# Optimization experiments

Measured on AMD Instinct MI355X. Metric: run time of the kernel, lower is better.

Reference implementation:

```python
import jax, jax.numpy as jnp
from jax import lax
import numpy as np

B, S, D, H = 64, 256, 1024, 1024
NEG = -1e9


def setup_inputs() -> dict:
    key = jax.random.key(0)
    ks = jax.random.split(key, 8)
    sd = 1.0 / np.sqrt(D)
    sh = 1.0 / np.sqrt(H + 1)
    return {
        "lstm_features": jax.random.normal(ks[0], (B, S, D), jnp.float32),
        "mask": jnp.ones((B, S), jnp.int32),
        "Wl": jax.random.normal(ks[1], (D, H), jnp.float32) * sd,
        "bl": jnp.zeros((H,), jnp.float32),
        "Wr": jax.random.normal(ks[2], (D, H), jnp.float32) * sd,
        "br": jnp.zeros((H,), jnp.float32),
        "Wbil": jax.random.normal(ks[3], (H + 1, H + 1), jnp.float32) * sh,
        "bbil": jnp.zeros((), jnp.float32),
    }


def _span_scores(lstm_features, Wl, bl, Wr, br, Wbil, bbil):
    # left/right MLPs: Linear + LeakyReLU(0.1) (dropout=0 at inference)
    lefts = jax.nn.leaky_relu(lstm_features @ Wl + bl, 0.1)   # [B,S,H]
    rights = jax.nn.leaky_relu(lstm_features @ Wr + br, 0.1)  # [B,S,H]
    ones = jnp.ones(lefts.shape[:-1] + (1,), lefts.dtype)
    l1 = jnp.concatenate([lefts, ones], axis=-1)   # [B,S,H+1] (use_input_biases=True)
    r1 = jnp.concatenate([rights, ones], axis=-1)
    # bilinear: l1 @ W @ r1^T + bias  -> [B,S,S]
    return jnp.einsum('bsh,hg,btg->bst', l1, Wbil, r1) + bbil


def _cky(scores):
    """CKY over one [S,S] score matrix. chart[i,j]=scores[i,j]+max_s chart[i,s]+chart[s+1,j];
    singleton spans score 0. Returns (chart, best-split table)."""
    n = scores.shape[0]
    idx = jnp.arange(n)
    m = jnp.arange(n - 1)  # split offsets
    chart0 = jnp.zeros((n, n), scores.dtype)
    split0 = jnp.zeros((n, n), jnp.int32)

    def step(carry, w):
        chart, split = carry
        j = idx + w
        jc = jnp.clip(j, 0, n - 1)
        li = jnp.clip(idx[:, None] + m[None, :], 0, n - 1)       # left end
        ri = jnp.clip(idx[:, None] + m[None, :] + 1, 0, n - 1)   # right start
        cand = chart[idx[:, None], li] + chart[ri, jc[:, None]]  # [n, n-1]
        valid = (m[None, :] < w) & (j[:, None] < n)
        cand = jnp.where(valid, cand, NEG)
        val = scores[idx, jc] + jnp.max(cand, axis=1)
        bsplit = (idx + jnp.argmax(cand, axis=1)).astype(jnp.int32)
        ok = j < n
        chart = chart.at[idx, jc].set(jnp.where(ok, val, chart[idx, jc]))
        split = split.at[idx, jc].set(jnp.where(ok, bsplit, split[idx, jc]))
        return (chart, split), None

    (chart, split), _ = lax.scan(step, (chart0, split0), jnp.arange(1, n))
    return chart, split


def _backtrack(split):
    """Extract the n-1 internal spans of the best tree (fixed-size stack, jit-safe)."""
    n = split.shape[0]
    stack = jnp.full((2 * n, 2), -1, jnp.int32).at[0].set(jnp.array([0, n - 1], jnp.int32))
    out = jnp.zeros((n, 2), jnp.int32)

    def body(t, state):
        def do_pop(st):
            stack, top, out, cnt = st
            ij = stack[top - 1]
            i, j = ij[0], ij[1]
            top = top - 1
            out = out.at[cnt].set(ij)
            cnt = cnt + 1
            s = split[i, j]
            stack = stack.at[top].set(jnp.stack([i, s]))          # left child
            top = top + (s > i).astype(jnp.int32)
            stack = stack.at[top].set(jnp.stack([s + 1, j]))      # right child
            top = top + (j > s + 1).astype(jnp.int32)
            return (stack, top, out, cnt)
        return lax.cond(state[1] > 0, do_pop, lambda s: s, state)

    state = (stack, jnp.int32(1), out, jnp.int32(0))
    _, _, out, _ = lax.fori_loop(0, n - 1, body, state)
    return out  # [n,2] (lefts, rights), zero-padded like torch.zeros in original


def reference(lstm_features, mask, Wl, bl, Wr, br, Wbil, bbil):
    scores = _span_scores(lstm_features, Wl, bl, Wr, br, Wbil, bbil)  # [B,S,S]
    _, split = jax.vmap(_cky)(scores)
    spans = jax.vmap(_backtrack)(split)  # [B,S,2]
    ret_lefts = spans[..., 0].astype(jnp.int64)
    ret_rights = spans[..., 1].astype(jnp.int64)
    return ret_lefts, ret_rights
```

## Files before the change

kernel.cpp:

```cpp
#include <hip/hip_runtime.h>
#include <cstdint>


#define Bb 64
#define Ss 256
#define Dd 1024
#define Hh 1024

typedef __attribute__((ext_vector_type(8))) _Float16 f16x8;
typedef __attribute__((ext_vector_type(4))) float f32x4;

__device__ __forceinline__ void split2(float x, unsigned short& h,
                                       unsigned short& l) {
  _Float16 hh = (_Float16)x;
  _Float16 ll = (_Float16)(x - (float)hh);
  h = __builtin_bit_cast(unsigned short, hh);
  l = __builtin_bit_cast(unsigned short, ll);
}

__device__ __forceinline__ void gl_lds16(const void* g, void* l) {
  __builtin_amdgcn_global_load_lds(
      (const __attribute__((address_space(1))) void*)g,
      (__attribute__((address_space(3))) void*)l, 16, 0, 0);
}

__global__ __launch_bounds__(256) void splitw_kernel(
    const float* __restrict__ W, int ldw, unsigned short* __restrict__ O,
    long long plane) {
  int idx = blockIdx.x * 256 + threadIdx.x;
  int n = idx >> 10, k = idx & 1023;
  float x = W[(long long)k * ldw + n];
  unsigned short h, l;
  split2(x, h, l);
  O[idx] = h;
  O[plane + idx] = l;
}

__global__ __launch_bounds__(256) void bilvec_kernel(
    const float* __restrict__ Wbil, float* __restrict__ brow,
    float* __restrict__ bcol, float* __restrict__ corner) {
  int i = blockIdx.x * 256 + threadIdx.x;
  brow[i] = Wbil[1024 * 1025 + i];
  bcol[i] = Wbil[i * 1025 + 1024];
  if (i == 0) corner[0] = Wbil[1024 * 1025 + 1024];
}

__device__ __forceinline__ void pack8(char* dst, const unsigned short* v) {
  uint4 u;
  u.x = (unsigned)v[0] | ((unsigned)v[1] << 16);
  u.y = (unsigned)v[2] | ((unsigned)v[3] << 16);
  u.z = (unsigned)v[4] | ((unsigned)v[5] << 16);
  u.w = (unsigned)v[6] | ((unsigned)v[7] << 16);
  *(uint4*)dst = u;
}

__device__ __forceinline__ void split_store16f(const float* xs, char* lds,
                                               int base, int wa0, int wa1) {
  unsigned short hs[16], ls[16];
#pragma unroll
  for (int i = 0; i < 16; ++i) split2(xs[i], hs[i], ls[i]);
  pack8(&lds[base + wa0], hs);
  pack8(&lds[base + wa1], hs + 8);
  pack8(&lds[base + 8192 + wa0], ls);
  pack8(&lds[base + 8192 + wa1], ls + 8);
}

#define MFMA4(afv, bh, blv, accs, nf)                                        \
  {                                                                          \
    _Pragma("unroll") for (int mf = 0; mf < 4; ++mf) accs[mf][nf] =          \
        __builtin_amdgcn_mfma_f32_16x16x32_f16(afv[0][mf], bh,               \
                                               accs[mf][nf], 0, 0, 0);       \
    _Pragma("unroll") for (int mf = 0; mf < 4; ++mf) accs[mf][nf] =          \
        __builtin_amdgcn_mfma_f32_16x16x32_f16(afv[0][mf], blv,              \
                                               accs[mf][nf], 0, 0, 0);       \
    _Pragma("unroll") for (int mf = 0; mf < 4; ++mf) accs[mf][nf] =          \
        __builtin_amdgcn_mfma_f32_16x16x32_f16(afv[1][mf], bh,               \
                                               accs[mf][nf], 0, 0, 0);       \
    _Pragma("unroll") for (int mf = 0; mf < 4; ++mf) accs[mf][nf] =          \
        __builtin_amdgcn_mfma_f32_16x16x32_f16(afv[1][mf], blv,              \
                                               accs[mf][nf], 0, 0, 0);       \
  }

template <bool LEAKY>
__global__ __launch_bounds__(256, 3) void gemm_mfma_kernel(
    const float* __restrict__ A, const unsigned short* __restrict__ Bsp,
    long long bplane, float* __restrict__ C0, float* __restrict__ C1,
    const float* __restrict__ bias0, const float* __restrict__ bias1) {
  const int m0 = blockIdx.y * 128;
  const int n0 = blockIdx.x * 128;
  __shared__ __align__(16) char lds[49152];
  const int t = threadIdx.x;
  const int L = t & 63, w = t >> 6, q = L >> 4, l15 = L & 15;

  const int ar = t >> 1, ah = t & 1;
  const float* aptr = A + (long long)(m0 + ar) * 1024 + ah * 16;
  const int phiA = ((ar >> 1) ^ (ar >> 3)) & 3;
  const int wa0 = ar * 64 + (((2 * ah + 0) ^ phiA) << 4);
  const int wa1 = ar * 64 + (((2 * ah + 1) ^ phiA) << 4);

  int offA0[4], offB0[4];
#pragma unroll
  for (int f = 0; f < 4; ++f) {
    int rowa = ((w & 1) << 6) + (f << 4) + l15;
    offA0[f] = rowa * 64 + ((q ^ (((rowa >> 1) ^ (rowa >> 3)) & 3)) << 4);
    int rowb = ((w >> 1) << 6) + (f << 4) + l15;
    offB0[f] = rowb * 64 + ((q ^ (((rowb >> 1) ^ (rowb >> 3)) & 3)) << 4);
  }

  const int lrow = L >> 2, lchk = L & 3;
  const unsigned short* bsrc[4];
  int bldso[4];
#pragma unroll
  for (int i = 0; i < 4; ++i) {
    int O = ((w << 2) + i) << 10;
    int s2 = O >> 13;
    int r = ((O & 8191) >> 6) + lrow;
    int phi = ((r >> 1) ^ (r >> 3)) & 3;
    bsrc[i] = Bsp + (long long)s2 * bplane + (long long)(n0 + r) * 1024 +
              ((lchk ^ phi) << 3);
    bldso[i] = O;
  }

  f32x4 acc[4][4];
#pragma unroll
  for (int i = 0; i < 4; ++i)
#pragma unroll
    for (int j = 0; j < 4; ++j) acc[i][j] = (f32x4){0.f, 0.f, 0.f, 0.f};

#pragma unroll
  for (int i = 0; i < 4; ++i) gl_lds16(bsrc[i], &lds[16384 + bldso[i]]);
  float4 a0 = *(const float4*)(aptr + 0);
  float4 a1 = *(const float4*)(aptr + 4);
  float4 a2 = *(const float4*)(aptr + 8);
  float4 a3 = *(const float4*)(aptr + 12);

  int cur = 0;
  for (int k0 = 0; k0 < 1024; k0 += 32) {
    {
      float xs[16] = {a0.x, a0.y, a0.z, a0.w, a1.x, a1.y, a1.z, a1.w,
                      a2.x, a2.y, a2.z, a2.w, a3.x, a3.y, a3.z, a3.w};
      split_store16f(xs, lds, 0, wa0, wa1);
    }
    asm volatile("s_waitcnt vmcnt(0) lgkmcnt(0)\n\ts_barrier" ::: "memory");
    if (k0 < 992) {
      a0 = *(const float4*)(aptr + k0 + 32);
      a1 = *(const float4*)(aptr + k0 + 36);
      a2 = *(const float4*)(aptr + k0 + 40);
      a3 = *(const float4*)(aptr + k0 + 44);
      const int bn = 16384 + ((cur ^ 1) << 14);
#pragma unroll
      for (int i = 0; i < 4; ++i)
        gl_lds16(bsrc[i] + k0 + 32, &lds[bn + bldso[i]]);
    }
    const int bb = 16384 + (cur << 14);
    f16x8 af[2][4];
#pragma unroll
    for (int s = 0; s < 2; ++s)
#pragma unroll
      for (int f = 0; f < 4; ++f)
        af[s][f] = *(const f16x8*)&lds[s * 8192 + offA0[f]];
#pragma unroll
    for (int nf = 0; nf < 4; ++nf) {
      f16x8 bh = *(const f16x8*)&lds[bb + offB0[nf]];
      f16x8 bl = *(const f16x8*)&lds[bb + 8192 + offB0[nf]];
      MFMA4(af, bh, bl, acc, nf);
    }
    asm volatile("s_waitcnt lgkmcnt(0)\n\ts_barrier" ::: "memory");
    cur ^= 1;
  }

  const bool isR = (n0 >= 1024);
  float* Co = isR ? C1 : C0;
  const float* bp = isR ? bias1 : bias0;
  const int nc0 = n0 & 1023;
#pragma unroll
  for (int nf = 0; nf < 4; ++nf) {
    int col = nc0 + ((w >> 1) << 6) + (nf << 4) + l15;
    float bz = bp[col];
#pragma unroll
    for (int mf = 0; mf < 4; ++mf) {
#pragma unroll
      for (int r = 0; r < 4; ++r) {
        int row = m0 + ((w & 1) << 6) + (mf << 4) + (q << 2) + r;
        float x = acc[mf][nf][r] + bz;
        if (LEAKY) x = (x > 0.f) ? x : 0.1f * x;
        Co[(long long)row * 1024 + col] = x;
      }
    }
  }
}

__global__ __launch_bounds__(256, 3) void gemmnt_mfma_kernel(
    const float* __restrict__ A, const float* __restrict__ B,
    float* __restrict__ C, const float* __restrict__ rowAdd,
    const float* __restrict__ scal) {
  const int bz = blockIdx.z;
  A += (long long)bz * 256 * 1024;
  B += (long long)bz * 256 * 1024;
  C += (long long)bz * 256 * 256;
  const int m0 = blockIdx.y * 128;
  const int n0 = blockIdx.x * 128;
  __shared__ __align__(16) char lds[32768];
  const int t = threadIdx.x;
  const int L = t & 63, w = t >> 6, q = L >> 4, l15 = L & 15;

  const int ar = t >> 1, ah = t & 1;
  const float* aptr = A + (long long)(m0 + ar) * 1024 + ah * 16;
  const float* bptr = B + (long long)(n0 + ar) * 1024 + ah * 16;
  const int phiA = ((ar >> 1) ^ (ar >> 3)) & 3;
  const int wa0 = ar * 64 + (((2 * ah + 0) ^ phiA) << 4);
  const int wa1 = ar * 64 + (((2 * ah + 1) ^ phiA) << 4);

  int offA0[4], offB0[4];
#pragma unroll
  for (int f = 0; f < 4; ++f) {
    int rowa = ((w & 1) << 6) + (f << 4) + l15;
    offA0[f] = rowa * 64 + ((q ^ (((rowa >> 1) ^ (rowa >> 3)) & 3)) << 4);
    int rowb = ((w >> 1) << 6) + (f << 4) + l15;
    offB0[f] =
        16384 + rowb * 64 + ((q ^ (((rowb >> 1) ^ (rowb >> 3)) & 3)) << 4);
  }

  f32x4 acc[4][4];
#pragma unroll
  for (int i = 0; i < 4; ++i)
#pragma unroll
    for (int j = 0; j < 4; ++j) acc[i][j] = (f32x4){0.f, 0.f, 0.f, 0.f};

  float4 a0 = *(const float4*)(aptr + 0);
  float4 a1 = *(const float4*)(aptr + 4);
  float4 a2 = *(const float4*)(aptr + 8);
  float4 a3 = *(const float4*)(aptr + 12);
  float4 b0 = *(const float4*)(bptr + 0);
  float4 b1 = *(const float4*)(bptr + 4);
  float4 b2 = *(const float4*)(bptr + 8);
  float4 b3 = *(const float4*)(bptr + 12);

  for (int k0 = 0; k0 < 1024; k0 += 32) {
    {
      float xs[16] = {a0.x, a0.y, a0.z, a0.w, a1.x, a1.y, a1.z, a1.w,
                      a2.x, a2.y, a2.z, a2.w, a3.x, a3.y, a3.z, a3.w};
      split_store16f(xs, lds, 0, wa0, wa1);
      float ys[16] = {b0.x, b0.y, b0.z, b0.w, b1.x, b1.y, b1.z, b1.w,
                      b2.x, b2.y, b2.z, b2.w, b3.x, b3.y, b3.z, b3.w};
      split_store16f(ys, lds, 16384, wa0, wa1);
    }
    asm volatile("s_waitcnt lgkmcnt(0)\n\ts_barrier" ::: "memory");
    if (k0 < 992) {
      a0 = *(const float4*)(aptr + k0 + 32);
      a1 = *(const float4*)(aptr + k0 + 36);
      a2 = *(const float4*)(aptr + k0 + 40);
      a3 = *(const float4*)(aptr + k0 + 44);
      b0 = *(const float4*)(bptr + k0 + 32);
      b1 = *(const float4*)(bptr + k0 + 36);
      b2 = *(const float4*)(bptr + k0 + 40);
      b3 = *(const float4*)(bptr + k0 + 44);
    }
    f16x8 af[2][4];
#pragma unroll
    for (int s = 0; s < 2; ++s)
#pragma unroll
      for (int f = 0; f < 4; ++f)
        af[s][f] = *(const f16x8*)&lds[s * 8192 + offA0[f]];
#pragma unroll
    for (int nf = 0; nf < 4; ++nf) {
      f16x8 bh = *(const f16x8*)&lds[offB0[nf]];
      f16x8 bl = *(const f16x8*)&lds[8192 + offB0[nf]];
      MFMA4(af, bh, bl, acc, nf);
    }
    asm volatile("s_waitcnt lgkmcnt(0)\n\ts_barrier" ::: "memory");
  }

  const float sc_add = scal[0];
#pragma unroll
  for (int mf = 0; mf < 4; ++mf) {
#pragma unroll
    for (int r = 0; r < 4; ++r) {
      int row = m0 + ((w & 1) << 6) + (mf << 4) + (q << 2) + r;
      float radd = sc_add + rowAdd[(long long)bz * 256 + row];
#pragma unroll
      for (int nf = 0; nf < 4; ++nf) {
        int col = n0 + ((w >> 1) << 6) + (nf << 4) + l15;
        C[(long long)row * 256 + col] = acc[mf][nf][r] + radd;
      }
    }
  }
}

__global__ __launch_bounds__(64) void colvec_kernel(
    const float* __restrict__ lefts, const float* __restrict__ bcol,
    const float* __restrict__ corner, float* __restrict__ tmpb) {
  int row = blockIdx.x;
  int lane = threadIdx.x;
  const float* a = lefts + (long long)row * Hh;
  float s = 0.f;
#pragma unroll
  for (int h = lane; h < Hh; h += 64) s = fmaf(a[h], bcol[h], s);
#pragma unroll
  for (int off = 32; off > 0; off >>= 1) s += __shfl_down(s, off, 64);
  if (lane == 0) tmpb[row] = s + corner[0];
}

__global__ __launch_bounds__(1024) void cky_kernel(
    const float* __restrict__ scores,
    uint8_t* __restrict__ Sws,
    int* __restrict__ out)
{
  const int b = blockIdx.x;
  const int t = threadIdx.x;
  const int n = Ss;
  const float* sc = scores + (long long)b * n * n;
  uint8_t* SP = Sws + (long long)b * 32896;

  __shared__ float Dch[32896];
  __shared__ float pv[2][2048];
  __shared__ uint8_t pmv[2][2048];
  __shared__ int stk[256];

  const int offT[16] = {0,    256,  511,  765,  1018, 1270, 1521, 1771,
                        2020, 2268, 2515, 2761, 3006, 3250, 3493, 3735};

  if (t < n) {
    out[b * n + t] = 0;
    out[Bb * n + b * n + t] = 0;
    Dch[t] = 0.f;
  }
  pv[1][t] = -3.0e38f;
  pv[1][t + 1024] = -3.0e38f;

  float PS[16];
  PS[0] = 0.f;
#pragma unroll
  for (int w = 1; w <= 15; ++w) {
    int ic = t;
    if (ic > 255 - w) ic = 255 - w;
    PS[w] = sc[ic * 257 + w];
  }
  asm volatile("s_waitcnt lgkmcnt(0)\n\ts_barrier" ::: "memory");

#pragma unroll
  for (int w = 1; w <= 15; ++w) {
    if (t < 256 - w) {
      float bb = Dch[offT[w - 1] + t + 1];
      int bm = 0;
#pragma unroll
      for (int m = 1; m < 15; ++m) {
        if (m >= w) break;
        float c = Dch[offT[m] + t] + Dch[offT[w - 1 - m] + t + m + 1];
        if (c > bb) { bb = c; bm = m; }
      }
      Dch[offT[w] + t] = PS[w] + bb;
      SP[offT[w] + t] = (uint8_t)bm;
    }
    asm volatile("s_waitcnt lgkmcnt(0)\n\ts_barrier" ::: "memory");
  }

  auto run_b = [&](int W0b, int pbuf) {
    const int cnv = n - W0b - 8;
    int jb, gb, u, delta;
    if (cnv > 128) {
      jb = 7 - (t >> 7);
      gb = 0;
      u = t & 127;
      delta = 128;
    } else {
      const int wid = t >> 6;
      jb = 7 - (wid >> 1);
      gb = wid & 1;
      u = t & 63;
      delta = (cnv > 64) ? 64 : 0;
    }
    const int Wb = W0b + 8 + jb;
    const int nvb = n - Wb;
    int cnt = W0b - jb - 8;
    if (cnt < 0) cnt = 0;
    const int mlo = jb + 8;
    int ml, mh;
    if (cnv > 128) {
      ml = mlo;
      mh = mlo + cnt;
    } else {
      const int per = (cnt + 1) >> 1;
      ml = mlo + gb * per;
      mh = mlo + cnt;
      int e = ml + per;
      if (e < mh) mh = e;
    }
    float b0 = -3.0e38f, b1 = -3.0e38f;
    int m0i = ml, m1i = ml;
    if (u < nvb && ml < mh) {
      int al = ml * n - ((ml * (ml - 1)) >> 1) + u;
      const int kr = Wb - 1 - ml;
      int ar = kr * n - ((kr * (kr - 1)) >> 1) + u + ml + 1;
      int dl = n - ml;
      int dr = n - Wb + ml + 1;
      if (delta) {
#pragma unroll 4
        for (int m = ml; m < mh; ++m) {
          float l0 = Dch[al], l1 = Dch[al + delta];
          float r0 = Dch[ar], r1 = Dch[ar + delta];
          float c0 = l0 + r0, c1 = l1 + r1;
          if (c0 > b0) { b0 = c0; m0i = m; }
          if (c1 > b1) { b1 = c1; m1i = m; }
          al += dl;
          ar -= dr;
          --dl;
          ++dr;
        }
      } else {
#pragma unroll 8
        for (int m = ml; m < mh; ++m) {
          float c = Dch[al] + Dch[ar];
          if (c > b0) { b0 = c; m0i = m; }
          al += dl;
          ar -= dr;
          --dl;
          ++dr;
        }
      }
    }
    const int slot = jb * 256 + gb * 128 + u;
    pv[pbuf][slot] = b0;
    pmv[pbuf][slot] = (uint8_t)m0i;
    if (delta) {
      pv[pbuf][slot + delta] = b1;
      pmv[pbuf][slot + delta] = (uint8_t)m1i;
    }
  };

  const int wv = t >> 6, lane = t & 63;
  const int tcell = 57 * wv + lane;

  float scA[8];
#pragma unroll
  for (int j = 0; j < 8; ++j) {
    const int Wn = 16 + j;
    int ic = tcell;
    if (ic > 255 - Wn) ic = 255 - Wn;
    scA[j] = sc[ic * 257 + Wn];
  }

  for (int s = 2; s <= 31; ++s) {
    const int W0 = 8 * s;
    const int nv1 = n - W0;
    const int pb = s & 1, po = pb ^ 1;
    const int nb = (nv1 + 56) / 57;

    float P8[8] = {0.f, 0.f, 0.f, 0.f, 0.f, 0.f, 0.f, 0.f};
    if (s < 31 && wv < nb) {
#pragma unroll
      for (int j = 0; j < 8; ++j) {
        const int Wn = W0 + 8 + j;
        int ic = tcell;
        if (ic > 255 - Wn) ic = 255 - Wn;
        if (ic < 0) ic = 0;
        P8[j] = sc[ic * 257 + Wn];
      }
    }

    if (wv < nb) {
      const int tc = (tcell < nv1) ? tcell : (nv1 - 1);
      const float* pvo = pv[po];
      const uint8_t* pmo = pmv[po];
      const bool RA = (nv1 > 128);
      int offPB[8], offCB[8];
#pragma unroll
      for (int d = 0; d < 8; ++d) {
        const int dg = W0 - 8 + d;
        offPB[d] = dg * 256 - ((dg * (dg - 1)) >> 1);
        const int cg = W0 + d;
        offCB[d] = cg * 256 - ((cg * (cg - 1)) >> 1);
      }
      float VAL[8];
#pragma unroll
      for (int j = 0; j < 8; ++j) {
        const int W = W0 + j;
        float bb;
        int bm = 0;
        if (j == 0) {
          bb = Dch[offPB[7] + tc + 1];
        } else {
          bb = __shfl_down(VAL[j - 1], 1, 64);
        }
#pragma unroll
        for (int m = 1; m < 8; ++m) {
          if (m >= j) break;
          float c = Dch[offT[m] + tc] + __shfl_down(VAL[j - 1 - m], m + 1, 64);
          if (c > bb) { bb = c; bm = m; }
        }
#pragma unroll
        for (int m2 = 0; m2 < 8; ++m2) {
          const int m = j + m2;
          if (m == 0) continue;
          float c = Dch[offT[m] + tc] + Dch[offPB[7 - m2] + tc + m + 1];
          if (c > bb) { bb = c; bm = m; }
        }
        if (RA) {
          const int sl = j * 256 + tc;
          float x = pvo[sl];
          if (x > bb) { bb = x; bm = pmo[sl]; }
        } else {
#pragma unroll
          for (int g = 0; g < 2; ++g) {
            const int sl = j * 256 + g * 128 + tc;
            float x = pvo[sl];
            if (x > bb) { bb = x; bm = pmo[sl]; }
          }
        }
#pragma unroll
        for (int d = 0; d < 8; ++d) {
          const int m = W0 - 8 + d;
          const int rp = j + 7 - d;
          float right = (rp == 0) ? 0.f : Dch[offT[rp] + tc + W - rp];
          float c = Dch[offPB[d] + tc] + right;
          if (c > bb) { bb = c; bm = m; }
        }
#pragma unroll
        for (int e = 0; e < 8; ++e) {
          if (e >= j) break;
          const int rp = j - 1 - e;
          float right = (rp == 0) ? 0.f : Dch[offT[rp] + tc + W - rp];
          float c = VAL[e] + right;
          if (c > bb) { bb = c; bm = W0 + e; }
        }
        VAL[j] = scA[j] + bb;
        if (lane <= 63 - j && tcell < nv1 - j) {
          Dch[offCB[j] + tcell] = VAL[j];
          SP[offCB[j] + tcell] = (uint8_t)bm;
        }
      }
    }

    if (s < 31) run_b(W0, pb);

    asm volatile("s_waitcnt lgkmcnt(0)\n\ts_barrier" ::: "memory");
#pragma unroll
    for (int j = 0; j < 8; ++j) scA[j] = P8[j];
  }

  asm volatile("s_waitcnt vmcnt(0) lgkmcnt(0)\n\ts_barrier" ::: "memory");
  uint8_t* spl = (uint8_t*)Dch;
  for (int idx = t; idx < 32896; idx += 1024) spl[idx] = SP[idx];
  asm volatile("s_waitcnt vmcnt(0) lgkmcnt(0)\n\ts_barrier" ::: "memory");
  if (t == 0) {
    int top = 0;
    stk[top++] = (0 << 16) | (n - 1);
    int cnt = 0;
    for (int step = 0; step < n - 1; ++step) {
      if (top > 0) {
        int ij = stk[--top];
        int ii = ij >> 16, jj = ij & 0xffff;
        out[b * n + cnt] = ii;
        out[Bb * n + b * n + cnt] = jj;
        ++cnt;
        int k = jj - ii;
        int s2 = ii + (int)spl[k * n - ((k * (k - 1)) >> 1) + ii];
        stk[top] = (ii << 16) | s2;
        if (s2 > ii) ++top;
        stk[top] = ((s2 + 1) << 16) | jj;
        if (jj > s2 + 1) ++top;
      }
    }
  }
}

extern "C" void kernel_launch(void* const* d_in, const int* in_sizes, int n_in,
                              void* d_out, int out_size, void* d_ws,
                              size_t ws_size, hipStream_t stream) {
  const float* X = (const float*)d_in[0];
  const float* Wl = (const float*)d_in[2];
  const float* bl = (const float*)d_in[3];
  const float* Wr = (const float*)d_in[4];
  const float* br = (const float*)d_in[5];
  const float* Wbil = (const float*)d_in[6];
  const float* bbil = (const float*)d_in[7];
  int* out = (int*)d_out;

  float* ws = (float*)d_ws;
  float* lefts = ws;
  float* rights = lefts + 16777216;
  float* tmpA = rights + 16777216;
  float* scoresP = tmpA + 16777216;
  float* tmpb = scoresP + 4194304;
  float* browp = tmpb + 16384;
  float* bcolp = browp + 1024;
  float* cornerp = bcolp + 1024;
  unsigned short* Wlrt = (unsigned short*)(cornerp + 4);
  unsigned short* Wct = Wlrt + 2LL * 2097152;
  uint8_t* SPp = (uint8_t*)(Wct + 2LL * 1048576);

  splitw_kernel<<<dim3(4096), 256, 0, stream>>>(Wl, 1024, Wlrt, 2097152);
  splitw_kernel<<<dim3(4096), 256, 0, stream>>>(Wr, 1024, Wlrt + 1048576,
                                                2097152);
  splitw_kernel<<<dim3(4096), 256, 0, stream>>>(Wbil, 1025, Wct, 1048576);
  bilvec_kernel<<<dim3(4), 256, 0, stream>>>(Wbil, browp, bcolp, cornerp);

  dim3 gLR(16, 128);
  gemm_mfma_kernel<true><<<gLR, 256, 0, stream>>>(X, Wlrt, 2097152LL, lefts,
                                                  rights, bl, br);

  colvec_kernel<<<dim3(16384), 64, 0, stream>>>(lefts, bcolp, cornerp, tmpb);

  dim3 gA(8, 128);
  gemm_mfma_kernel<false><<<gA, 256, 0, stream>>>(lefts, Wct, 1048576LL, tmpA,
                                                  tmpA, browp, browp);

  dim3 g3(2, 2, 64);
  gemmnt_mfma_kernel<<<g3, 256, 0, stream>>>(tmpA, rights, scoresP, tmpb,
                                             bbil);

  cky_kernel<<<dim3(Bb), dim3(1024), 0, stream>>>(scoresP, SPp, out);
}
```

Baseline: 863.4 us.

## Pre-split activations into fp16 hi/lo planes and load A fragments directly from global

Result: slower. 948.2 us (+9.8%).

```diff
diff --git a/kernel.cpp b/kernel.cpp
--- a/kernel.cpp
+++ b/kernel.cpp
@@ -34,6 +34,25 @@
   split2(x, h, l);
   O[idx] = h;
   O[plane + idx] = l;
+}
+
+__global__ __launch_bounds__(256) void splitx_kernel(
+    const float* __restrict__ X, unsigned short* __restrict__ O,
+    long long plane) {
+  long long i4 = ((long long)blockIdx.x * 256 + threadIdx.x) * 4;
+  float4 v = *(const float4*)(X + i4);
+  unsigned short h[4], l[4];
+  split2(v.x, h[0], l[0]);
+  split2(v.y, h[1], l[1]);
+  split2(v.z, h[2], l[2]);
+  split2(v.w, h[3], l[3]);
+  uint2 hp, lp;
+  hp.x = (unsigned)h[0] | ((unsigned)h[1] << 16);
+  hp.y = (unsigned)h[2] | ((unsigned)h[3] << 16);
+  lp.x = (unsigned)l[0] | ((unsigned)l[1] << 16);
+  lp.y = (unsigned)l[2] | ((unsigned)l[3] << 16);
+  *(uint2*)(O + i4) = hp;
+  *(uint2*)(O + plane + i4) = lp;
 }
 
 __global__ __launch_bounds__(256) void bilvec_kernel(
@@ -80,6 +99,115 @@
         __builtin_amdgcn_mfma_f32_16x16x32_f16(afv[1][mf], blv,              \
                                                accs[mf][nf], 0, 0, 0);       \
   }
+
+template <bool LEAKY>
+__global__ __launch_bounds__(256, 3) void gemm_ar_kernel(
+    const unsigned short* __restrict__ Asp, long long aplane,
+    const unsigned short* __restrict__ Bsp, long long bplane,
+    float* __restrict__ C0, float* __restrict__ C1,
+    const float* __restrict__ bias0, const float* __restrict__ bias1) {
+  const int m0 = blockIdx.y * 128;
+  const int n0 = blockIdx.x * 128;
+  __shared__ __align__(16) char lds[32768];
+  const int t = threadIdx.x;
+  const int L = t & 63, w = t >> 6, q = L >> 4, l15 = L & 15;
+
+  int offB0[4];
+#pragma unroll
+  for (int f = 0; f < 4; ++f) {
+    int rowb = ((w >> 1) << 6) + (f << 4) + l15;
+    offB0[f] = rowb * 64 + ((q ^ (((rowb >> 1) ^ (rowb >> 3)) & 3)) << 4);
+  }
+
+  const unsigned short* aps[2][4];
+#pragma unroll
+  for (int f = 0; f < 4; ++f) {
+    int rowa = ((w & 1) << 6) + (f << 4) + l15;
+#pragma unroll
+    for (int s = 0; s < 2; ++s)
+      aps[s][f] = Asp + (long long)s * aplane +
+                  (long long)(m0 + rowa) * 1024 + q * 8;
+  }
+
+  const int lrow = L >> 2, lchk = L & 3;
+  const unsigned short* bsrc[4];
+  int bldso[4];
+#pragma unroll
+  for (int i = 0; i < 4; ++i) {
+    int O = ((w << 2) + i) << 10;
+    int s2 = O >> 13;
+    int r = ((O & 8191) >> 6) + lrow;
+    int phi = ((r >> 1) ^ (r >> 3)) & 3;
+    bsrc[i] = Bsp + (long long)s2 * bplane + (long long)(n0 + r) * 1024 +
+              ((lchk ^ phi) << 3);
+    bldso[i] = O;
+  }
+
+  f32x4 acc[4][4];
+#pragma unroll
+  for (int i = 0; i < 4; ++i)
+#pragma unroll
+    for (int j = 0; j < 4; ++j) acc[i][j] = (f32x4){0.f, 0.f, 0.f, 0.f};
+
+#pragma unroll
+  for (int i = 0; i < 4; ++i) gl_lds16(bsrc[i], &lds[bldso[i]]);
+  f16x8 af[2][4], afn[2][4];
+#pragma unroll
+  for (int s = 0; s < 2; ++s)
+#pragma unroll
+    for (int f = 0; f < 4; ++f) af[s][f] = *(const f16x8*)(aps[s][f]);
+  asm volatile("s_waitcnt vmcnt(0)\n\ts_barrier" ::: "memory");
+
+  int cur = 0;
+  for (int k0 = 0; k0 < 1024; k0 += 32) {
+    if (k0 < 992) {
+      const int bn = (cur ^ 1) << 14;
+#pragma unroll
+      for (int i = 0; i < 4; ++i)
+        gl_lds16(bsrc[i] + k0 + 32, &lds[bn + bldso[i]]);
+#pragma unroll
+      for (int s = 0; s < 2; ++s)
+#pragma unroll
+        for (int f = 0; f < 4; ++f)
+          afn[s][f] = *(const f16x8*)(aps[s][f] + k0 + 32);
+    }
+    const int bbase = cur << 14;
+#pragma unroll
+    for (int nf = 0; nf < 4; ++nf) {
+      f16x8 bh = *(const f16x8*)&lds[bbase + offB0[nf]];
+      f16x8 bl = *(const f16x8*)&lds[bbase + 8192 + offB0[nf]];
+      MFMA4(af, bh, bl, acc, nf);
+    }
+    asm volatile("s_waitcnt vmcnt(0) lgkmcnt(0)\n\ts_barrier" ::: "memory");
+    if (k0 < 992) {
+#pragma unroll
+      for (int s = 0; s < 2; ++s)
+#pragma unroll
+        for (int f = 0; f < 4; ++f) af[s][f] = afn[s][f];
+    }
+    cur ^= 1;
+  }
+
+  const bool isR = (n0 >= 1024);
+  float* Co = isR ? C1 : C0;
+  const float* bp = isR ? bias1 : bias0;
+  const int nc0 = n0 & 1023;
+#pragma unroll
+  for (int nf = 0; nf < 4; ++nf) {
+    int col = nc0 + ((w >> 1) << 6) + (nf << 4) + l15;
+    float bz = bp[col];
+#pragma unroll
+    for (int mf = 0; mf < 4; ++mf) {
+#pragma unroll
+      for (int r = 0; r < 4; ++r) {
+        int row = m0 + ((w & 1) << 6) + (mf << 4) + (q << 2) + r;
+        float x = acc[mf][nf][r] + bz;
+        if (LEAKY) x = (x > 0.f) ? x : 0.1f * x;
+        Co[(long long)row * 1024 + col] = x;
+      }
+    }
+  }
+}
 
 template <bool LEAKY>
 __global__ __launch_bounds__(256, 3) void gemm_mfma_kernel(
@@ -589,15 +717,18 @@
   unsigned short* Wct = Wlrt + 2LL * 2097152;
   uint8_t* SPp = (uint8_t*)(Wct + 2LL * 1048576);
 
+  unsigned short* Xsp = (unsigned short*)tmpA;
+
   splitw_kernel<<<dim3(4096), 256, 0, stream>>>(Wl, 1024, Wlrt, 2097152);
   splitw_kernel<<<dim3(4096), 256, 0, stream>>>(Wr, 1024, Wlrt + 1048576,
                                                 2097152);
   splitw_kernel<<<dim3(4096), 256, 0, stream>>>(Wbil, 1025, Wct, 1048576);
   bilvec_kernel<<<dim3(4), 256, 0, stream>>>(Wbil, browp, bcolp, cornerp);
+  splitx_kernel<<<dim3(16384), 256, 0, stream>>>(X, Xsp, 16777216LL);
 
   dim3 gLR(16, 128);
-  gemm_mfma_kernel<true><<<gLR, 256, 0, stream>>>(X, Wlrt, 2097152LL, lefts,
-                                                  rights, bl, br);
+  gemm_ar_kernel<true><<<gLR, 256, 0, stream>>>(
+      Xsp, 16777216LL, Wlrt, 2097152LL, lefts, rights, bl, br);
 
   colvec_kernel<<<dim3(16384), 64, 0, stream>>>(lefts, bcolp, cornerp, tmpb);
 
```
